# Performance work log

Measured on AMD Instinct MI355X. Metric: run time of the kernel, lower is better.

Reference implementation:

```python
import jax, jax.numpy as jnp
import numpy as np


def _get_pairs(top_k_centers):
    """Returns (p0, p1) int32 arrays of shape [B, S]: for each object a, the
    IoU-best partner a', ordered so the larger-L1 box comes first (as in source)."""
    cx, cy, h, w = jnp.split(top_k_centers, 4, axis=-1)  # [B,S,1] each, cxcyhw
    box = jnp.concatenate([cx - 0.5 * w, cy - 0.5 * h, cx + 0.5 * w, cy + 0.5 * h], axis=-1)  # [B,S,4] xyxy
    S = box.shape[1]
    b1 = box[:, :, None, :]  # [B,S,1,4]
    b2 = box[:, None, :, :]  # [B,1,S,4]
    inter_mins = jnp.maximum(b1[..., :2], b2[..., :2])
    inter_maxs = jnp.maximum(b1[..., 2:], b2[..., 2:])  # NOTE: source uses maximum here (kept faithful)
    inter_wh = jnp.clip(inter_maxs - inter_mins, 0.0)
    inter_area = inter_wh[..., 0] * inter_wh[..., 1]  # [B,S,S]
    area = (box[..., 2] - box[..., 0]) * (box[..., 3] - box[..., 1])  # [B,S]
    union = area[:, :, None] + area[:, None, :] - inter_area
    iou = inter_area / union - jnp.eye(S, dtype=inter_area.dtype)
    partner = jnp.argmax(iou, axis=-1)  # [B,S] int
    self_idx = jnp.broadcast_to(jnp.arange(S), partner.shape)
    l1 = jnp.abs(box[..., 2] - box[..., 0]) + jnp.abs(box[..., 3] - box[..., 1])  # [B,S]
    l1_partner = jnp.take_along_axis(l1, partner, axis=-1)
    keep = l1 >= l1_partner  # larger-L1 element goes first
    p0 = jnp.where(keep, self_idx, partner)
    p1 = jnp.where(keep, partner, self_idx)
    return p0, p1


def _gather_pair(a2, p):
    # a2: [B,H,S,S]; p: [B,S]. out[b,h,a,c] = a2[b,h,p[b,a],p[b,c]]
    rows = jnp.take_along_axis(a2, p[:, None, :, None], axis=2)
    return jnp.take_along_axis(rows, p[:, None, None, :], axis=3)


def setup_inputs() -> dict:
    key = jax.random.key(0)
    kq, kk, kv, kc = jax.random.split(key, 4)
    B, H, S, D = 8, 8, 1024, 64
    return {
        "query": jax.random.normal(kq, (B, H, S, D), dtype=jnp.float32),
        "key": jax.random.normal(kk, (B, H, S, D), dtype=jnp.float32),
        "value": jax.random.normal(kv, (B, H, S, D), dtype=jnp.float32),
        "top_k_centers": jax.random.uniform(kc, (B, S, 4), dtype=jnp.float32),
    }


def reference(query, key, value, top_k_centers):
    B, H, S, D = query.shape
    p0, p1 = _get_pairs(top_k_centers)
    # A2(a,b) = <q_{pi_a}, k_{pi_b}> + <q_{pi_a'}, k_{pi_b'}>
    a2 = jnp.einsum('bhqd,bhkd->bhqk', query, key)  # [B,H,S,S]
    scores = (_gather_pair(a2, p0) + _gather_pair(a2, p1)) * (1.0 / np.sqrt(2.0 * D))
    attn = jax.nn.softmax(scores, axis=-1)
    o2 = jnp.einsum('bhqk,bhkd->bhqd', attn, value)  # [B,H,S,D]
    return o2.transpose(0, 2, 1, 3).reshape(B, S, H * D)
```

## Files before the change

kernel.cpp:

```cpp
#include <hip/hip_runtime.h>
#include <hip/hip_bf16.h>

#define B_ 8
#define H_ 8
#define S_ 1024
#define D_ 64
#define QT 128
#define KT 64
#define NT (S_ / KT)

typedef float f32x16 __attribute__((ext_vector_type(16)));
typedef short s16x8 __attribute__((ext_vector_type(8)));
typedef unsigned int u32;

#define CSCALE ((float)(1.4426950408889634 / 11.313708498984761))

static __device__ __forceinline__ unsigned short f2bf(float f) {
    union { float f; unsigned u; } v; v.f = f;
    unsigned r = v.u + 0x7FFF + ((v.u >> 16) & 1);
    return (unsigned short)(r >> 16);
}

static __device__ __forceinline__ u32 cvtpk(float lo, float hi) {
    u32 r;
    asm("v_cvt_pk_bf16_f32 %0, %1, %2" : "=v"(r) : "v"(lo), "v"(hi));
    return r;
}

static __device__ __forceinline__ void glds16(const void* g, void* l) {
    __builtin_amdgcn_global_load_lds(
        (const __attribute__((address_space(1))) unsigned int*)(uintptr_t)g,
        (__attribute__((address_space(3))) unsigned int*)(unsigned)(uintptr_t)l,
        16, 0, 0);
}

__global__ __launch_bounds__(256) void pairs_kernel(const float* __restrict__ centers,
                                                    int* __restrict__ p0,
                                                    int* __restrict__ p1) {
#pragma clang fp contract(off)
    __shared__ float x0s[S_], y0s[S_], x1s[S_], y1s[S_], areas[S_], l1s[S_];
    const int b = blockIdx.y;
    const int t = threadIdx.x;
    for (int idx = t; idx < S_; idx += 256) {
        const float4 c = *reinterpret_cast<const float4*>(centers + ((size_t)b * S_ + idx) * 4);
        const float cx = c.x, cy = c.y, hh = c.z, ww = c.w;
        const float x0 = cx - 0.5f * ww;
        const float y0 = cy - 0.5f * hh;
        const float x1 = cx + 0.5f * ww;
        const float y1 = cy + 0.5f * hh;
        x0s[idx] = x0; y0s[idx] = y0; x1s[idx] = x1; y1s[idx] = y1;
        areas[idx] = (x1 - x0) * (y1 - y0);
        l1s[idx] = fabsf(x1 - x0) + fabsf(y1 - y0);
    }
    __syncthreads();
    const int i = blockIdx.x * 32 + (t >> 3);
    const int c8 = t & 7;
    const float x0i = x0s[i], y0i = y0s[i], x1i = x1s[i], y1i = y1s[i], ai = areas[i];
    float best = -1e38f; int arg = 0;
    const int j0 = c8 * 128;
    for (int j = j0; j < j0 + 128; ++j) {
        float wx = fmaxf(x1i, x1s[j]) - fmaxf(x0i, x0s[j]);
        float wy = fmaxf(y1i, y1s[j]) - fmaxf(y0i, y0s[j]);
        wx = fmaxf(wx, 0.0f);
        wy = fmaxf(wy, 0.0f);
        const float inter = wx * wy;
        const float uni = (ai + areas[j]) - inter;
        float v = inter / uni;
        if (j == i) v = v - 1.0f;
        if (v > best) { best = v; arg = j; }
    }
    #pragma unroll
    for (int m = 1; m <= 4; m <<= 1) {
        const float ob = __shfl_xor(best, m);
        const int oa = __shfl_xor(arg, m);
        if (ob > best || (ob == best && oa < arg)) { best = ob; arg = oa; }
    }
    if (c8 == 0) {
        const int partner = arg;
        const float l1i = l1s[i], l1p = l1s[partner];
        const int keep = (l1i >= l1p) ? 1 : 0;
        p0[b * S_ + i] = keep ? i : partner;
        p1[b * S_ + i] = keep ? partner : i;
    }
}

__global__ __launch_bounds__(256) void prep_kv(const float* __restrict__ k,
                                               const float* __restrict__ v,
                                               const int* __restrict__ p0,
                                               const int* __restrict__ p1,
                                               unsigned short* __restrict__ Kg,
                                               unsigned short* __restrict__ Vt) {
    __shared__ float tile[64][65];
    const int bh = blockIdx.y;
    const int b = bh >> 3;
    const int s0 = blockIdx.x * 64;
    const int t = threadIdx.x;
    const int w = t >> 6, lane = t & 63;
    {
        const float* kp = k + (size_t)bh * S_ * D_;
        const int* p0b = p0 + b * S_;
        const int* p1b = p1 + b * S_;
        for (int i = 0; i < 16; ++i) {
            const int s = s0 + w * 16 + i;
            const int i0 = p0b[s], i1 = p1b[s];
            const float a0 = kp[(size_t)i0 * D_ + lane];
            const float a1 = kp[(size_t)i1 * D_ + lane];
            const int sw = (s & 7) << 3;
            unsigned short* row = Kg + ((size_t)bh * S_ + s) * 128;
            row[lane ^ sw] = f2bf(a0);
            row[(64 + lane) ^ sw] = f2bf(a1);
        }
    }
    {
        const float* vp = v + ((size_t)bh * S_ + s0) * D_;
        const int row = t >> 2, cpart = (t & 3) * 16;
        for (int jj = 0; jj < 4; ++jj) {
            const float4 x = *reinterpret_cast<const float4*>(&vp[(size_t)row * D_ + cpart + jj * 4]);
            tile[row][cpart + jj * 4 + 0] = x.x;
            tile[row][cpart + jj * 4 + 1] = x.y;
            tile[row][cpart + jj * 4 + 2] = x.z;
            tile[row][cpart + jj * 4 + 3] = x.w;
        }
        __syncthreads();
        const int d = t >> 2;
        unsigned short* orow = Vt + ((size_t)bh * 64 + d) * S_ + s0;
        for (int cc = 0; cc < 2; ++cc) {
            const int chunk = (t & 3) * 2 + cc;
            unsigned short hh[8];
            for (int e = 0; e < 8; ++e) hh[e] = f2bf(tile[chunk * 8 + e][d]);
            const int chunk2 = chunk ^ (d & 7);
            *reinterpret_cast<s16x8*>(&orow[chunk2 * 8]) = *reinterpret_cast<s16x8*>(hh);
        }
    }
}

__global__ __launch_bounds__(256, 2) void attn_kernel(const float* __restrict__ q,
                                                      const unsigned short* __restrict__ Kg,
                                                      const unsigned short* __restrict__ Vt,
                                                      const int* __restrict__ p0,
                                                      const int* __restrict__ p1,
                                                      float* __restrict__ out) {
    __shared__ __align__(16) unsigned short Ks[2][KT][128];
    __shared__ __align__(16) unsigned short Vs[2][D_][KT];

    const int tid = threadIdx.x;
    const int w = tid >> 6;
    const int lane = tid & 63;
    const int qc = lane & 31;
    const int hi = lane >> 5;
    const int qtile = blockIdx.x;
    const int bh = blockIdx.y;
    const int b = bh >> 3;
    const int h = bh & 7;

    const float* qp = q + (size_t)bh * S_ * D_;
    const unsigned short* KgB = Kg + (size_t)bh * S_ * 128;
    const unsigned short* VtB = Vt + (size_t)bh * D_ * S_;

    {
        const int rK = lane >> 4;
        const size_t cK = (size_t)(lane & 15) * 8;
        #pragma unroll
        for (int qq = 0; qq < 4; ++qq)
            glds16(KgB + ((size_t)((w * 4 + qq) * 4 + rK)) * 128 + cK, &Ks[0][(w * 4 + qq) * 4][0]);
        const int rV = lane >> 3;
        const size_t cV = (size_t)(lane & 7) * 8;
        #pragma unroll
        for (int qq = 0; qq < 2; ++qq)
            glds16(VtB + ((size_t)((w * 2 + qq) * 8 + rV)) * S_ + cV, &Vs[0][(w * 2 + qq) * 8][0]);
    }

    s16x8 qf[8];
    {
        const int qr = qtile * QT + w * 32 + qc;
        const int i0 = p0[b * S_ + qr], i1 = p1[b * S_ + qr];
        #pragma unroll
        for (int p = 0; p < 8; ++p) {
            const int k0 = 16 * p + 8 * hi;
            const float* src = (p < 4) ? (qp + (size_t)i0 * D_ + k0)
                                       : (qp + (size_t)i1 * D_ + (k0 - 64));
            const float4 f0 = *reinterpret_cast<const float4*>(src);
            const float4 f1 = *reinterpret_cast<const float4*>(src + 4);
            union { u32 u[4]; s16x8 v; } pk;
            pk.u[0] = cvtpk(f0.x * CSCALE, f0.y * CSCALE);
            pk.u[1] = cvtpk(f0.z * CSCALE, f0.w * CSCALE);
            pk.u[2] = cvtpk(f1.x * CSCALE, f1.y * CSCALE);
            pk.u[3] = cvtpk(f1.z * CSCALE, f1.w * CSCALE);
            qf[p] = pk.v;
        }
    }
    __syncthreads();

    f32x16 oacc0 = {}, oacc1 = {};
    float m_run = -1e30f, l_run = 0.0f;
    const int swz = qc & 7;

    for (int kt = 0; kt < NT; ++kt) {
        const int bf = kt & 1;
        if (kt + 1 < NT) {
            const int rK = lane >> 4;
            const size_t cK = (size_t)(lane & 15) * 8;
            const size_t kbase = (size_t)((kt + 1) * KT) * 128;
            #pragma unroll
            for (int qq = 0; qq < 4; ++qq)
                glds16(KgB + kbase + ((size_t)((w * 4 + qq) * 4 + rK)) * 128 + cK,
                       &Ks[bf ^ 1][(w * 4 + qq) * 4][0]);
            const int rV = lane >> 3;
            const size_t cV = (size_t)((kt + 1) * KT) + (size_t)(lane & 7) * 8;
            #pragma unroll
            for (int qq = 0; qq < 2; ++qq)
                glds16(VtB + ((size_t)((w * 2 + qq) * 8 + rV)) * S_ + cV,
                       &Vs[bf ^ 1][(w * 2 + qq) * 8][0]);
        }

        f32x16 st0 = {}, st1 = {};
        #pragma unroll
        for (int p = 0; p < 8; ++p) {
            const int ch = (2 * p + hi) ^ swz;
            const s16x8 kf0 = *reinterpret_cast<const s16x8*>(&Ks[bf][qc][ch * 8]);
            st0 = __builtin_amdgcn_mfma_f32_32x32x16_bf16(kf0, qf[p], st0, 0, 0, 0);
            const s16x8 kf1 = *reinterpret_cast<const s16x8*>(&Ks[bf][32 + qc][ch * 8]);
            st1 = __builtin_amdgcn_mfma_f32_32x32x16_bf16(kf1, qf[p], st1, 0, 0, 0);
        }

        float t16[16];
        #pragma unroll
        for (int i = 0; i < 16; ++i) t16[i] = fmaxf(st0[i], st1[i]);
        #pragma unroll
        for (int i = 0; i < 8; ++i) t16[i] = fmaxf(t16[i], t16[i + 8]);
        #pragma unroll
        for (int i = 0; i < 4; ++i) t16[i] = fmaxf(t16[i], t16[i + 4]);
        float mx = fmaxf(fmaxf(t16[0], t16[1]), fmaxf(t16[2], t16[3]));
        mx = fmaxf(mx, __shfl_xor(mx, 32));
        const float mn = fmaxf(m_run, mx);
        const float alpha = exp2f(m_run - mn);
        m_run = mn;
        #pragma unroll
        for (int i = 0; i < 16; ++i) {
            st0[i] = exp2f(st0[i] - mn);
            st1[i] = exp2f(st1[i] - mn);
        }
        float a16[16];
        #pragma unroll
        for (int i = 0; i < 16; ++i) a16[i] = st0[i] + st1[i];
        #pragma unroll
        for (int i = 0; i < 8; ++i) a16[i] += a16[i + 8];
        #pragma unroll
        for (int i = 0; i < 4; ++i) a16[i] += a16[i + 4];
        float ps = (a16[0] + a16[1]) + (a16[2] + a16[3]);
        ps += __shfl_xor(ps, 32);
        l_run = l_run * alpha + ps;
        oacc0 *= alpha;
        oacc1 *= alpha;

        u32 U0[8], U1[8];
        #pragma unroll
        for (int i = 0; i < 8; ++i) {
            U0[i] = cvtpk(st0[2 * i], st0[2 * i + 1]);
            U1[i] = cvtpk(st1[2 * i], st1[2 * i + 1]);
        }

        #pragma unroll
        for (int s = 0; s < 4; ++s) {
            const u32* Ut = (s < 2) ? U0 : U1;
            const int a = 4 * (s & 1);
            const u32 sendA = hi ? Ut[a] : Ut[a + 2];
            const u32 recvA = __shfl_xor(sendA, 32);
            const u32 w0 = hi ? recvA : Ut[a];
            const u32 w2 = hi ? Ut[a + 2] : recvA;
            const u32 sendB = hi ? Ut[a + 1] : Ut[a + 3];
            const u32 recvB = __shfl_xor(sendB, 32);
            const u32 w1 = hi ? recvB : Ut[a + 1];
            const u32 w3 = hi ? Ut[a + 3] : recvB;
            union { u32 u[4]; s16x8 v; } pf;
            pf.u[0] = w0; pf.u[1] = w1; pf.u[2] = w2; pf.u[3] = w3;
            const int ch = (2 * s + hi) ^ swz;
            const s16x8 vf0 = *reinterpret_cast<const s16x8*>(&Vs[bf][qc][ch * 8]);
            oacc0 = __builtin_amdgcn_mfma_f32_32x32x16_bf16(vf0, pf.v, oacc0, 0, 0, 0);
            const s16x8 vf1 = *reinterpret_cast<const s16x8*>(&Vs[bf][32 + qc][ch * 8]);
            oacc1 = __builtin_amdgcn_mfma_f32_32x32x16_bf16(vf1, pf.v, oacc1, 0, 0, 0);
        }
        __syncthreads();
    }

    const float invl = 1.0f / l_run;
    const int qrg = qtile * QT + w * 32 + qc;
    float* orow = out + ((size_t)b * S_ + qrg) * (H_ * D_) + h * D_;
    #pragma unroll
    for (int rq = 0; rq < 4; ++rq) {
        const float4 v0 = { oacc0[4 * rq] * invl, oacc0[4 * rq + 1] * invl,
                            oacc0[4 * rq + 2] * invl, oacc0[4 * rq + 3] * invl };
        *reinterpret_cast<float4*>(orow + 8 * rq + 4 * hi) = v0;
        const float4 v1 = { oacc1[4 * rq] * invl, oacc1[4 * rq + 1] * invl,
                            oacc1[4 * rq + 2] * invl, oacc1[4 * rq + 3] * invl };
        *reinterpret_cast<float4*>(orow + 32 + 8 * rq + 4 * hi) = v1;
    }
}

extern "C" void kernel_launch(void* const* d_in, const int* in_sizes, int n_in,
                              void* d_out, int out_size, void* d_ws, size_t ws_size,
                              hipStream_t stream) {
    (void)in_sizes; (void)n_in; (void)out_size; (void)ws_size;
    const float* q = (const float*)d_in[0];
    const float* k = (const float*)d_in[1];
    const float* v = (const float*)d_in[2];
    const float* c = (const float*)d_in[3];
    float* out = (float*)d_out;
    int* p0 = (int*)d_ws;
    int* p1 = p0 + B_ * S_;
    unsigned short* Kg = (unsigned short*)((char*)d_ws + 65536);
    unsigned short* Vt = Kg + (size_t)B_ * H_ * S_ * 128;
    pairs_kernel<<<dim3(32, 8), 256, 0, stream>>>(c, p0, p1);
    prep_kv<<<dim3(16, 64), 256, 0, stream>>>(k, v, p0, p1, Kg, Vt);
    attn_kernel<<<dim3(8, 64), 256, 0, stream>>>(q, Kg, Vt, p0, p1, out);
}
```

Before: 82.97 us.

## Triple-buffer K/V tiles, lazy softmax rescale, vectorize K gather, remap grids

The attention kernel moves from double to triple buffering of K/V in LDS, with explicit vmcnt waits and one barrier per iteration instead of a trailing __syncthreads. It also raises wave priority around the MFMA blocks and only rescales the running max, sum and accumulators when the new max exceeds the old by more than 8 (exp2 domain). prep_kv now gathers K rows with float4 loads and writes 16-byte packed bf16 chunks instead of scalar stores. Both launches become 1D grids with an index remap that groups blocks sharing a batch across heads. The extra LDS buffer may lower occupancy, and the lazy rescale lets exp values reach up to 2^8 before normalization.

After: 81.66 us. No clear change (-1.6%).

```diff
diff --git a/kernel.cpp b/kernel.cpp
--- a/kernel.cpp
+++ b/kernel.cpp
@@ -91,24 +91,32 @@
                                                unsigned short* __restrict__ Kg,
                                                unsigned short* __restrict__ Vt) {
     __shared__ float tile[64][65];
-    const int bh = blockIdx.y;
+    const int gid = blockIdx.x;
+    const int stile = (gid >> 3) & 15;
+    const int bh = ((gid >> 7) << 3) | (gid & 7);
     const int b = bh >> 3;
-    const int s0 = blockIdx.x * 64;
+    const int s0 = stile * 64;
     const int t = threadIdx.x;
-    const int w = t >> 6, lane = t & 63;
     {
         const float* kp = k + (size_t)bh * S_ * D_;
         const int* p0b = p0 + b * S_;
         const int* p1b = p1 + b * S_;
-        for (int i = 0; i < 16; ++i) {
-            const int s = s0 + w * 16 + i;
+        const int chunk = t & 15;
+        const int rsub = t >> 4;
+        for (int it = 0; it < 4; ++it) {
+            const int s = s0 + it * 16 + rsub;
             const int i0 = p0b[s], i1 = p1b[s];
-            const float a0 = kp[(size_t)i0 * D_ + lane];
-            const float a1 = kp[(size_t)i1 * D_ + lane];
-            const int sw = (s & 7) << 3;
+            const float* src = (chunk < 8) ? (kp + (size_t)i0 * D_ + chunk * 8)
+                                           : (kp + (size_t)i1 * D_ + (chunk - 8) * 8);
+            const float4 f0 = *reinterpret_cast<const float4*>(src);
+            const float4 f1 = *reinterpret_cast<const float4*>(src + 4);
+            union { u32 u[4]; s16x8 v; } pk;
+            pk.u[0] = cvtpk(f0.x, f0.y);
+            pk.u[1] = cvtpk(f0.z, f0.w);
+            pk.u[2] = cvtpk(f1.x, f1.y);
+            pk.u[3] = cvtpk(f1.z, f1.w);
             unsigned short* row = Kg + ((size_t)bh * S_ + s) * 128;
-            row[lane ^ sw] = f2bf(a0);
-            row[(64 + lane) ^ sw] = f2bf(a1);
+            *reinterpret_cast<s16x8*>(row + (size_t)(chunk ^ (s & 7)) * 8) = pk.v;
         }
     }
     {
@@ -140,35 +148,23 @@
                                                       const int* __restrict__ p0,
                                                       const int* __restrict__ p1,
                                                       float* __restrict__ out) {
-    __shared__ __align__(16) unsigned short Ks[2][KT][128];
-    __shared__ __align__(16) unsigned short Vs[2][D_][KT];
+    __shared__ __align__(16) unsigned short Ks[3][KT][128];
+    __shared__ __align__(16) unsigned short Vs[3][D_][KT];
 
     const int tid = threadIdx.x;
     const int w = tid >> 6;
     const int lane = tid & 63;
     const int qc = lane & 31;
     const int hi = lane >> 5;
-    const int qtile = blockIdx.x;
-    const int bh = blockIdx.y;
+    const int gid = blockIdx.x;
+    const int qtile = (gid >> 3) & 7;
+    const int bh = ((gid >> 6) << 3) | (gid & 7);
     const int b = bh >> 3;
     const int h = bh & 7;
 
     const float* qp = q + (size_t)bh * S_ * D_;
     const unsigned short* KgB = Kg + (size_t)bh * S_ * 128;
     const unsigned short* VtB = Vt + (size_t)bh * D_ * S_;
-
-    {
-        const int rK = lane >> 4;
-        const size_t cK = (size_t)(lane & 15) * 8;
-        #pragma unroll
-        for (int qq = 0; qq < 4; ++qq)
-            glds16(KgB + ((size_t)((w * 4 + qq) * 4 + rK)) * 128 + cK, &Ks[0][(w * 4 + qq) * 4][0]);
-        const int rV = lane >> 3;
-        const size_t cV = (size_t)(lane & 7) * 8;
-        #pragma unroll
-        for (int qq = 0; qq < 2; ++qq)
-            glds16(VtB + ((size_t)((w * 2 + qq) * 8 + rV)) * S_ + cV, &Vs[0][(w * 2 + qq) * 8][0]);
-    }
 
     s16x8 qf[8];
     {
@@ -189,39 +185,50 @@
             qf[p] = pk.v;
         }
     }
-    __syncthreads();
+
+    const int rK = lane >> 4;
+    const size_t cK = (size_t)(lane & 15) * 8;
+    const int rV = lane >> 3;
+    const size_t cV8 = (size_t)(lane & 7) * 8;
+    auto STAGE = [&](int kt, int bf) {
+        const size_t kbase = (size_t)(kt * KT) * 128;
+        #pragma unroll
+        for (int qq = 0; qq < 4; ++qq)
+            glds16(KgB + kbase + ((size_t)((w * 4 + qq) * 4 + rK)) * 128 + cK,
+                   &Ks[bf][(w * 4 + qq) * 4][0]);
+        #pragma unroll
+        for (int qq = 0; qq < 2; ++qq)
+            glds16(VtB + ((size_t)((w * 2 + qq) * 8 + rV)) * S_ + (size_t)(kt * KT) + cV8,
+                   &Vs[bf][(w * 2 + qq) * 8][0]);
+    };
+    STAGE(0, 0);
+    STAGE(1, 1);
 
     f32x16 oacc0 = {}, oacc1 = {};
     float m_run = -1e30f, l_run = 0.0f;
     const int swz = qc & 7;
+    int cur = 0, nxt2 = 2;
 
     for (int kt = 0; kt < NT; ++kt) {
-        const int bf = kt & 1;
-        if (kt + 1 < NT) {
-            const int rK = lane >> 4;
-            const size_t cK = (size_t)(lane & 15) * 8;
-            const size_t kbase = (size_t)((kt + 1) * KT) * 128;
-            #pragma unroll
-            for (int qq = 0; qq < 4; ++qq)
-                glds16(KgB + kbase + ((size_t)((w * 4 + qq) * 4 + rK)) * 128 + cK,
-                       &Ks[bf ^ 1][(w * 4 + qq) * 4][0]);
-            const int rV = lane >> 3;
-            const size_t cV = (size_t)((kt + 1) * KT) + (size_t)(lane & 7) * 8;
-            #pragma unroll
-            for (int qq = 0; qq < 2; ++qq)
-                glds16(VtB + ((size_t)((w * 2 + qq) * 8 + rV)) * S_ + cV,
-                       &Vs[bf ^ 1][(w * 2 + qq) * 8][0]);
-        }
+        if (kt + 1 < NT) asm volatile("s_waitcnt vmcnt(6)" ::: "memory");
+        else             asm volatile("s_waitcnt vmcnt(0)" ::: "memory");
+        __builtin_amdgcn_s_barrier();
+        if (kt + 2 < NT) STAGE(kt + 2, nxt2);
+
+        const unsigned short(*KsC)[128] = Ks[cur];
+        const unsigned short(*VsC)[KT] = Vs[cur];
 
         f32x16 st0 = {}, st1 = {};
+        __builtin_amdgcn_s_setprio(1);
         #pragma unroll
         for (int p = 0; p < 8; ++p) {
             const int ch = (2 * p + hi) ^ swz;
-            const s16x8 kf0 = *reinterpret_cast<const s16x8*>(&Ks[bf][qc][ch * 8]);
+            const s16x8 kf0 = *reinterpret_cast<const s16x8*>(&KsC[qc][ch * 8]);
             st0 = __builtin_amdgcn_mfma_f32_32x32x16_bf16(kf0, qf[p], st0, 0, 0, 0);
-            const s16x8 kf1 = *reinterpret_cast<const s16x8*>(&Ks[bf][32 + qc][ch * 8]);
+            const s16x8 kf1 = *reinterpret_cast<const s16x8*>(&KsC[32 + qc][ch * 8]);
             st1 = __builtin_amdgcn_mfma_f32_32x32x16_bf16(kf1, qf[p], st1, 0, 0, 0);
         }
+        __builtin_amdgcn_s_setprio(0);
 
         float t16[16];
         #pragma unroll
@@ -232,13 +239,18 @@
         for (int i = 0; i < 4; ++i) t16[i] = fmaxf(t16[i], t16[i + 4]);
         float mx = fmaxf(fmaxf(t16[0], t16[1]), fmaxf(t16[2], t16[3]));
         mx = fmaxf(mx, __shfl_xor(mx, 32));
-        const float mn = fmaxf(m_run, mx);
-        const float alpha = exp2f(m_run - mn);
-        m_run = mn;
+        if (!__all(mx <= m_run + 8.0f)) {
+            const float mn = fmaxf(m_run, mx);
+            const float alpha = exp2f(m_run - mn);
+            m_run = mn;
+            l_run *= alpha;
+            oacc0 *= alpha;
+            oacc1 *= alpha;
+        }
         #pragma unroll
         for (int i = 0; i < 16; ++i) {
-            st0[i] = exp2f(st0[i] - mn);
-            st1[i] = exp2f(st1[i] - mn);
+            st0[i] = exp2f(st0[i] - m_run);
+            st1[i] = exp2f(st1[i] - m_run);
         }
         float a16[16];
         #pragma unroll
@@ -249,9 +261,7 @@
         for (int i = 0; i < 4; ++i) a16[i] += a16[i + 4];
         float ps = (a16[0] + a16[1]) + (a16[2] + a16[3]);
         ps += __shfl_xor(ps, 32);
-        l_run = l_run * alpha + ps;
-        oacc0 *= alpha;
-        oacc1 *= alpha;
+        l_run += ps;
 
         u32 U0[8], U1[8];
         #pragma unroll
@@ -275,12 +285,15 @@
             union { u32 u[4]; s16x8 v; } pf;
             pf.u[0] = w0; pf.u[1] = w1; pf.u[2] = w2; pf.u[3] = w3;
             const int ch = (2 * s + hi) ^ swz;
-            const s16x8 vf0 = *reinterpret_cast<const s16x8*>(&Vs[bf][qc][ch * 8]);
+            __builtin_amdgcn_s_setprio(1);
+            const s16x8 vf0 = *reinterpret_cast<const s16x8*>(&VsC[qc][ch * 8]);
             oacc0 = __builtin_amdgcn_mfma_f32_32x32x16_bf16(vf0, pf.v, oacc0, 0, 0, 0);
-            const s16x8 vf1 = *reinterpret_cast<const s16x8*>(&Vs[bf][32 + qc][ch * 8]);
+            const s16x8 vf1 = *reinterpret_cast<const s16x8*>(&VsC[32 + qc][ch * 8]);
             oacc1 = __builtin_amdgcn_mfma_f32_32x32x16_bf16(vf1, pf.v, oacc1, 0, 0, 0);
-        }
-        __syncthreads();
+            __builtin_amdgcn_s_setprio(0);
+        }
+        cur = (cur + 1 == 3) ? 0 : cur + 1;
+        nxt2 = (nxt2 + 1 == 3) ? 0 : nxt2 + 1;
     }
 
     const float invl = 1.0f / l_run;
@@ -311,6 +324,6 @@
     unsigned short* Kg = (unsigned short*)((char*)d_ws + 65536);
     unsigned short* Vt = Kg + (size_t)B_ * H_ * S_ * 128;
     pairs_kernel<<<dim3(32, 8), 256, 0, stream>>>(c, p0, p1);
-    prep_kv<<<dim3(16, 64), 256, 0, stream>>>(k, v, p0, p1, Kg, Vt);
-    attn_kernel<<<dim3(8, 64), 256, 0, stream>>>(q, Kg, Vt, p0, p1, out);
-}
+    prep_kv<<<dim3(1024), 256, 0, stream>>>(k, v, p0, p1, Kg, Vt);
+    attn_kernel<<<dim3(512), 256, 0, stream>>>(q, Kg, Vt, p0, p1, out);
+}
```
